# Performance work log

Hardware: AMD Instinct MI355X
Metric: run time of the kernel (lower is better)

## Reference

```python
import jax, jax.numpy as jnp
import numpy as np

MAX_ANS_LEN = 30  # init kwarg max_ans_len
EPS = 1e-8        # torch CosineSimilarity eps (norm clamp)
NEG_INF = jnp.float32(-jnp.inf)


def _per_example(seq, sep):
    # seq: [S, H] float, sep: [2] int (sep0, sep1)
    S, H = seq.shape
    sep0, sep1 = sep[0], sep[1]
    q1 = seq[1]                      # [H]
    q2 = seq[sep0 - 1]               # [H]
    # cos(cat(a,b), cat(q1,q2)) = (a.q1 + b.q2) / (sqrt(|a|^2+|b|^2) * sqrt(|q1|^2+|q2|^2))
    qnorm = jnp.sqrt(jnp.sum(q1 * q1) + jnp.sum(q2 * q2))
    dot1 = seq @ q1                  # [S] start-token numerator part
    dot2 = seq @ q2                  # [S] end-token numerator part
    nsq = jnp.sum(seq * seq, axis=1) # [S] squared norms

    i = jnp.arange(S)[:, None]               # [S,1] start index
    d = jnp.arange(MAX_ANS_LEN)[None, :]      # [1,W] band offset
    jraw = i + d                              # [S,W] end index (unclipped)
    j = jnp.clip(jraw, 0, S - 1)

    num = dot1[:, None] + dot2[j]                         # [S,W]
    denom = jnp.maximum(jnp.sqrt(nsq[:, None] + nsq[j]), EPS) * jnp.maximum(qnorm, EPS)
    sim = num / denom                                     # [S,W]

    valid = (i >= sep0 + 1) & (i < sep1) & (jraw < sep1)  # banded window mask
    sim_m = jnp.where(valid, sim, NEG_INF)

    start_max = jnp.max(sim_m, axis=1)        # [S]
    arg = jnp.argmax(sim_m, axis=1)           # [S]
    end_idx = jnp.clip(jnp.arange(S) + arg, 0, S - 1)
    row_valid = jnp.any(valid, axis=1)        # [S]

    start_logits = jnp.where(row_valid, start_max, 0.0)
    # end logit at each chosen end index = max over starts selecting that end (scatter-max)
    endv = jnp.full((S,), NEG_INF, dtype=seq.dtype).at[end_idx].max(
        jnp.where(row_valid, start_max, NEG_INF))
    end_logits = jnp.where(jnp.isneginf(endv), 0.0, endv)

    # null-answer heuristic: flip sign if max is not > mean + std (torch std is ddof=1)
    def _mean_std(x):
        m = jnp.mean(x)
        s = jnp.sqrt(jnp.sum((x - m) ** 2) / (S - 1))
        return m, s
    max_logit = jnp.max(start_logits)
    ms, ss = _mean_std(start_logits)
    me, se = _mean_std(end_logits)
    flip = (max_logit < ms + ss) | (max_logit < me + se)

    def _neg(x):
        return jnp.where(x == 0, jnp.asarray(-0.001, x.dtype), -x)
    start_out = jnp.where(flip, _neg(start_logits), start_logits)
    end_out = jnp.where(flip, _neg(end_logits), end_logits)
    return start_out, end_out


def setup_inputs() -> dict:
    key = jax.random.key(0)
    k1, k2, k3 = jax.random.split(key, 3)
    B, S, H = 8, 2048, 2048
    sequence_outputs = jax.random.normal(k1, (B, S, H), dtype=jnp.float32)
    sep0 = jax.random.randint(k2, (B,), 32, 128)
    sep1 = jax.random.randint(k3, (B,), 1024, S - 1)
    idxs = jnp.stack([sep0, sep1], axis=1).astype(jnp.int64)
    return {"sequence_outputs": sequence_outputs, "idxs": idxs}


def reference(sequence_outputs, idxs):
    start_logits, end_logits = jax.vmap(_per_example)(sequence_outputs, idxs)
    return start_logits, end_logits
```

## Files before the change

### kernel.cpp

```cpp
#include <hip/hip_runtime.h>
#include <hip/hip_bf16.h>

#define SEQ 2048
#define HID 2048
#define NB  8
#define WMAX 30
#define SLAB 16
#define EPSF 1e-8f
#define ENC_NEGINF 0x007fffffu
#define NSEG ((size_t)NB * SEQ)


__device__ __forceinline__ float dot4(float4 a, float4 b) {
    return a.x * b.x + a.y * b.y + a.z * b.z + a.w * b.w;
}

__global__ __launch_bounds__(512)
void k1_dots(const float* __restrict__ seq, const int* __restrict__ idxs,
             float* __restrict__ ws) {
    __shared__ float4 q1s[HID / 4];
    __shared__ float4 q2s[HID / 4];

    int bid = blockIdx.x;
    int b = bid >> 7;
    int rbase = (bid & 127) * SLAB;
    int t = threadIdx.x;

    int sep0 = idxs[2 * b], sep1 = idxs[2 * b + 1];

    bool needed = (rbase == 0) || (rbase + SLAB > sep0 - 1 && rbase < sep1);
    if (!needed) return;

    const float4* q1p = (const float4*)(seq + ((size_t)b * SEQ + 1) * HID);
    const float4* q2p = (const float4*)(seq + ((size_t)b * SEQ + (sep0 - 1)) * HID);
    q1s[t] = q1p[t];
    q2s[t] = q2p[t];
    __syncthreads();

    int w = t >> 6, lane = t & 63;
    int iA = rbase + w;
    int iB = iA + 8;
    const float4* rpA = (const float4*)(seq + ((size_t)b * SEQ + iA) * HID);
    const float4* rpB = (const float4*)(seq + ((size_t)b * SEQ + iB) * HID);

    float a1 = 0.f, a2 = 0.f, a3 = 0.f;
    float c1 = 0.f, c2 = 0.f, c3 = 0.f;
#pragma unroll
    for (int k = 0; k < 8; ++k) {
        float4 vA = rpA[k * 64 + lane];
        float4 vB = rpB[k * 64 + lane];
        float4 x  = q1s[k * 64 + lane];
        float4 y  = q2s[k * 64 + lane];
        a1 += dot4(vA, x); a2 += dot4(vA, y); a3 += dot4(vA, vA);
        c1 += dot4(vB, x); c2 += dot4(vB, y); c3 += dot4(vB, vB);
    }
#pragma unroll
    for (int off = 32; off; off >>= 1) {
        a1 += __shfl_xor(a1, off);
        a2 += __shfl_xor(a2, off);
        a3 += __shfl_xor(a3, off);
        c1 += __shfl_xor(c1, off);
        c2 += __shfl_xor(c2, off);
        c3 += __shfl_xor(c3, off);
    }
    if (lane == 0) {
        size_t oA = (size_t)b * SEQ + iA;
        size_t oB = (size_t)b * SEQ + iB;
        ws[oA] = a1;
        ws[NSEG + oA] = a2;
        ws[2 * NSEG + oA] = a3;
        ws[oB] = c1;
        ws[NSEG + oB] = c2;
        ws[2 * NSEG + oB] = c3;
    }
}

__device__ __forceinline__ unsigned enc_f(float f) {
    unsigned u = __float_as_uint(f);
    return (u & 0x80000000u) ? ~u : (u | 0x80000000u);
}
__device__ __forceinline__ float dec_f(unsigned k) {
    unsigned u = (k & 0x80000000u) ? (k ^ 0x80000000u) : ~k;
    return __uint_as_float(u);
}

__global__ __launch_bounds__(1024)
void k2_all(const float* __restrict__ ws, const int* __restrict__ idxs,
            float* __restrict__ out) {
    __shared__ float d2s[SEQ];
    __shared__ float nss[SEQ];
    __shared__ unsigned evs[SEQ];
    __shared__ float red[5][16];

    int b = blockIdx.x;
    int t = threadIdx.x;
    int sep0 = idxs[2 * b], sep1 = idxs[2 * b + 1];

    const float* dot1 = ws + (size_t)b * SEQ;
    const float* dot2 = ws + NSEG + (size_t)b * SEQ;
    const float* nsq  = ws + 2 * NSEG + (size_t)b * SEQ;

#pragma unroll
    for (int r = 0; r < 2; ++r) {
        int ii = t + r * 1024;
        d2s[ii] = dot2[ii];
        nss[ii] = nsq[ii];
        evs[ii] = ENC_NEGINF;
    }
    __syncthreads();

    float invq = 1.0f / fmaxf(sqrtf(nss[1] + nss[sep0 - 1]), EPSF);

    float slog[2];
#pragma unroll
    for (int r = 0; r < 2; ++r) {
        int ii = t + r * 1024;
        bool range_ok = (ii >= sep0 + 1) && (ii < sep1);
        float d1 = dot1[ii];
        float ni = nss[ii];
        float best = -__builtin_inff();
        int arg = 0;
        bool any = false;
#pragma unroll
        for (int d = 0; d < WMAX; ++d) {
            int jraw = ii + d;
            if (range_ok && jraw < sep1) {
                float num = d1 + d2s[jraw];
                float sim = num * rsqrtf(ni + nss[jraw]) * invq;
                if (sim > best) { best = sim; arg = d; }
                any = true;
            }
        }
        slog[r] = any ? best : 0.0f;
        if (any) {
            int e = ii + arg;
            if (e > SEQ - 1) e = SEQ - 1;
            atomicMax(&evs[e], enc_f(best));
        }
    }
    __syncthreads();

    float elog[2];
#pragma unroll
    for (int r = 0; r < 2; ++r) {
        int ii = t + r * 1024;
        unsigned k = evs[ii];
        elog[r] = (k == ENC_NEGINF) ? 0.0f : dec_f(k);
    }

    float ssum = 0.f, ssq = 0.f, esum = 0.f, esq = 0.f, smax = -__builtin_inff();
#pragma unroll
    for (int r = 0; r < 2; ++r) {
        ssum += slog[r]; ssq += slog[r] * slog[r];
        esum += elog[r]; esq += elog[r] * elog[r];
        smax = fmaxf(smax, slog[r]);
    }
#pragma unroll
    for (int off = 32; off; off >>= 1) {
        ssum += __shfl_xor(ssum, off);
        ssq  += __shfl_xor(ssq,  off);
        esum += __shfl_xor(esum, off);
        esq  += __shfl_xor(esq,  off);
        smax = fmaxf(smax, __shfl_xor(smax, off));
    }
    int lane = t & 63, w = t >> 6;
    if (lane == 0) {
        red[0][w] = ssum; red[1][w] = ssq; red[2][w] = esum;
        red[3][w] = esq;  red[4][w] = smax;
    }
    __syncthreads();

    float S0 = 0.f, S1 = 0.f, E0 = 0.f, E1 = 0.f, MX = -__builtin_inff();
#pragma unroll
    for (int k = 0; k < 16; ++k) {
        S0 += red[0][k]; S1 += red[1][k]; E0 += red[2][k];
        E1 += red[3][k]; MX = fmaxf(MX, red[4][k]);
    }
    float ms = S0 / SEQ;
    float ss = sqrtf(fmaxf(S1 - SEQ * ms * ms, 0.f) / (SEQ - 1));
    float me = E0 / SEQ;
    float se = sqrtf(fmaxf(E1 - SEQ * me * me, 0.f) / (SEQ - 1));
    bool flip = (MX < ms + ss) || (MX < me + se);

#pragma unroll
    for (int r = 0; r < 2; ++r) {
        int ii = t + r * 1024;
        float so = slog[r], eo = elog[r];
        if (flip) {
            so = (so == 0.f) ? -0.001f : -so;
            eo = (eo == 0.f) ? -0.001f : -eo;
        }
        out[(size_t)b * SEQ + ii] = so;
        out[NSEG + (size_t)b * SEQ + ii] = eo;
    }
}

extern "C" void kernel_launch(void* const* d_in, const int* in_sizes, int n_in,
                              void* d_out, int out_size, void* d_ws, size_t ws_size,
                              hipStream_t stream) {
    const float* seq = (const float*)d_in[0];
    const int* idxs = (const int*)d_in[1];
    float* out = (float*)d_out;
    float* ws = (float*)d_ws;

    k1_dots<<<NB * 128, 512, 0, stream>>>(seq, idxs, ws);
    k2_all<<<NB, 1024, 0, stream>>>(ws, idxs, out);
}
```

Measured before the change: 33.38 us.

## Split band scan into a 64-block kernel with global atomics and a finalize kernel

The banded similarity scan moves out of the single per-batch 1024-thread block into a separate kernel with 64 blocks of 256 threads, each staging its tile plus halo of dot2/nsq in shared memory as float2. End logits go through global atomicMax on a zero-initialised workspace array set by a memset. A second small kernel reads the start and end logits back and does the reductions and sign flip. The scan gains more parallelism, at the cost of an extra memset, an extra launch, global atomics and a round trip through memory.

After: 38.21 us. +14.5%, slower.

```diff
diff --git a/kernel.cpp b/kernel.cpp
--- a/kernel.cpp
+++ b/kernel.cpp
@@ -7,7 +7,6 @@
 #define WMAX 30
 #define SLAB 16
 #define EPSF 1e-8f
-#define ENC_NEGINF 0x007fffffu
 #define NSEG ((size_t)NB * SEQ)
 
 
@@ -84,68 +83,76 @@
     return __uint_as_float(u);
 }
 
-__global__ __launch_bounds__(1024)
-void k2_all(const float* __restrict__ ws, const int* __restrict__ idxs,
-            float* __restrict__ out) {
-    __shared__ float d2s[SEQ];
-    __shared__ float nss[SEQ];
-    __shared__ unsigned evs[SEQ];
-    __shared__ float red[5][16];
-
-    int b = blockIdx.x;
+__global__ __launch_bounds__(256)
+void k2a_band(const float* __restrict__ ws, const int* __restrict__ idxs) {
+    __shared__ float2 s2[256 + 32];
+
+    int blk = blockIdx.x;
+    int b = blk >> 3;
+    int base = (blk & 7) * 256;
     int t = threadIdx.x;
-    int sep0 = idxs[2 * b], sep1 = idxs[2 * b + 1];
 
     const float* dot1 = ws + (size_t)b * SEQ;
     const float* dot2 = ws + NSEG + (size_t)b * SEQ;
     const float* nsq  = ws + 2 * NSEG + (size_t)b * SEQ;
-
+    float* slog       = (float*)(ws + 3 * NSEG) + (size_t)b * SEQ;
+    unsigned* endv    = (unsigned*)(ws + 4 * NSEG) + (size_t)b * SEQ;
+
+    int g0 = base + t;
+    s2[t] = make_float2(dot2[g0], nsq[g0]);
+    if (t < 32) {
+        int g1 = base + 256 + t;
+        int gc = g1 > SEQ - 1 ? SEQ - 1 : g1;
+        s2[256 + t] = make_float2(dot2[gc], nsq[gc]);
+    }
+    __syncthreads();
+
+    int sep0 = idxs[2 * b], sep1 = idxs[2 * b + 1];
+    float invq = 1.0f / fmaxf(sqrtf(nsq[1] + nsq[sep0 - 1]), EPSF);
+
+    int i = base + t;
+    bool range_ok = (i >= sep0 + 1) && (i < sep1);
+    float d1 = dot1[i];
+    float ni = s2[t].y;
+
+    float best = -__builtin_inff();
+    int arg = 0;
+    bool any = false;
+#pragma unroll
+    for (int d = 0; d < WMAX; ++d) {
+        int jraw = i + d;
+        if (range_ok && jraw < sep1) {
+            float2 v = s2[t + d];
+            float sim = (d1 + v.x) * rsqrtf(ni + v.y) * invq;
+            if (sim > best) { best = sim; arg = d; }
+            any = true;
+        }
+    }
+    slog[i] = any ? best : 0.0f;
+    if (any) {
+        int e = i + arg;
+        if (e > SEQ - 1) e = SEQ - 1;
+        atomicMax(&endv[e], enc_f(best));
+    }
+}
+
+__global__ __launch_bounds__(1024)
+void k2b_fin(const float* __restrict__ ws, float* __restrict__ out) {
+    __shared__ float red[5][16];
+
+    int b = blockIdx.x;
+    int t = threadIdx.x;
+
+    const float* slogp = (const float*)(ws + 3 * NSEG) + (size_t)b * SEQ;
+    const unsigned* ev = (const unsigned*)(ws + 4 * NSEG) + (size_t)b * SEQ;
+
+    float slog[2], elog[2];
 #pragma unroll
     for (int r = 0; r < 2; ++r) {
-        int ii = t + r * 1024;
-        d2s[ii] = dot2[ii];
-        nss[ii] = nsq[ii];
-        evs[ii] = ENC_NEGINF;
-    }
-    __syncthreads();
-
-    float invq = 1.0f / fmaxf(sqrtf(nss[1] + nss[sep0 - 1]), EPSF);
-
-    float slog[2];
-#pragma unroll
-    for (int r = 0; r < 2; ++r) {
-        int ii = t + r * 1024;
-        bool range_ok = (ii >= sep0 + 1) && (ii < sep1);
-        float d1 = dot1[ii];
-        float ni = nss[ii];
-        float best = -__builtin_inff();
-        int arg = 0;
-        bool any = false;
-#pragma unroll
-        for (int d = 0; d < WMAX; ++d) {
-            int jraw = ii + d;
-            if (range_ok && jraw < sep1) {
-                float num = d1 + d2s[jraw];
-                float sim = num * rsqrtf(ni + nss[jraw]) * invq;
-                if (sim > best) { best = sim; arg = d; }
-                any = true;
-            }
-        }
-        slog[r] = any ? best : 0.0f;
-        if (any) {
-            int e = ii + arg;
-            if (e > SEQ - 1) e = SEQ - 1;
-            atomicMax(&evs[e], enc_f(best));
-        }
-    }
-    __syncthreads();
-
-    float elog[2];
-#pragma unroll
-    for (int r = 0; r < 2; ++r) {
-        int ii = t + r * 1024;
-        unsigned k = evs[ii];
-        elog[r] = (k == ENC_NEGINF) ? 0.0f : dec_f(k);
+        int i = t + r * 1024;
+        slog[r] = slogp[i];
+        unsigned k = ev[i];
+        elog[r] = (k == 0u) ? 0.0f : dec_f(k);
     }
 
     float ssum = 0.f, ssq = 0.f, esum = 0.f, esq = 0.f, smax = -__builtin_inff();
@@ -184,14 +191,14 @@
 
 #pragma unroll
     for (int r = 0; r < 2; ++r) {
-        int ii = t + r * 1024;
+        int i = t + r * 1024;
         float so = slog[r], eo = elog[r];
         if (flip) {
             so = (so == 0.f) ? -0.001f : -so;
             eo = (eo == 0.f) ? -0.001f : -eo;
         }
-        out[(size_t)b * SEQ + ii] = so;
-        out[NSEG + (size_t)b * SEQ + ii] = eo;
+        out[(size_t)b * SEQ + i] = so;
+        out[NSEG + (size_t)b * SEQ + i] = eo;
     }
 }
 
@@ -202,7 +209,10 @@
     const int* idxs = (const int*)d_in[1];
     float* out = (float*)d_out;
     float* ws = (float*)d_ws;
-
+    unsigned* endv = (unsigned*)(ws + 4 * NSEG);
+
+    hipMemsetAsync(endv, 0, NSEG * sizeof(unsigned), stream);
     k1_dots<<<NB * 128, 512, 0, stream>>>(seq, idxs, ws);
-    k2_all<<<NB, 1024, 0, stream>>>(ws, idxs, out);
-}
+    k2a_band<<<NB * 8, 256, 0, stream>>>(ws, idxs);
+    k2b_fin<<<NB, 1024, 0, stream>>>(ws, out);
+}
```
